# Kernel tuning notes

Hardware: AMD Instinct MI355X
Metric: run time of the kernel (lower is better)

Reference implementation:

```python
import jax, jax.numpy as jnp
import numpy as np

B, T, D_IN = 2048, 26, 512
H = 512          # hidden_size
E = 256          # num_char_embeddings
C = 97           # num_class
S = 32           # num_steps = batch_max_length + 1


def setup_inputs() -> dict:
    key = jax.random.key(0)
    ks = jax.random.split(key, 16)
    sc = lambda n: 1.0 / np.sqrt(n)
    inp = {
        "batch_H": jax.random.normal(ks[0], (B, T, D_IN), jnp.float32),
        "text": jax.random.randint(ks[1], (B, S), 0, C),
        # attention cell params
        "W_i2h": jax.random.normal(ks[2], (H, D_IN), jnp.float32) * sc(D_IN),
        "W_h2h": jax.random.normal(ks[3], (H, H), jnp.float32) * sc(H),
        "b_h2h": jax.random.normal(ks[4], (H,), jnp.float32) * sc(H),
        "w_score": jax.random.normal(ks[5], (1, H), jnp.float32) * sc(H),
        # LSTMCell params (gate order: i, f, g, o)
        "W_ih": jax.random.normal(ks[6], (4 * H, D_IN + E), jnp.float32) * sc(D_IN + E),
        "W_hh": jax.random.normal(ks[7], (4 * H, H), jnp.float32) * sc(H),
        "b_ih": jax.random.normal(ks[8], (4 * H,), jnp.float32) * sc(H),
        "b_hh": jax.random.normal(ks[9], (4 * H,), jnp.float32) * sc(H),
        # generator + char embedding
        "W_gen": jax.random.normal(ks[10], (C, H), jnp.float32) * sc(H),
        "b_gen": jax.random.normal(ks[11], (C,), jnp.float32) * sc(H),
        "emb_table": jax.random.normal(ks[12], (C, E), jnp.float32),
    }
    return inp


def _decode(batch_H, text, W_i2h, W_h2h, b_h2h, w_score,
            W_ih, W_hh, b_ih, b_hh, emb_table):
    # i2h(batch_H) is constant across steps -> hoist out of the loop
    Hp = jnp.einsum('btd,hd->bth', batch_H, W_i2h)          # [B,T,H]
    char_embs = emb_table[text]                              # [B,S,E]
    h0 = jnp.zeros((batch_H.shape[0], H), batch_H.dtype)
    c0 = jnp.zeros_like(h0)

    def step(carry, ce):
        h, c = carry
        ph = h @ W_h2h.T + b_h2h                             # [B,H]
        e = jnp.tanh(Hp + ph[:, None, :]) @ w_score[0]       # [B,T]
        alpha = jax.nn.softmax(e, axis=1)                    # [B,T]
        context = jnp.einsum('bt,btd->bd', alpha, batch_H)   # [B,D_IN]
        x = jnp.concatenate([context, ce], axis=1)           # [B,D_IN+E]
        gates = x @ W_ih.T + b_ih + h @ W_hh.T + b_hh        # [B,4H]
        i, f, g, o = jnp.split(gates, 4, axis=1)
        c_new = jax.nn.sigmoid(f) * c + jax.nn.sigmoid(i) * jnp.tanh(g)
        h_new = jax.nn.sigmoid(o) * jnp.tanh(c_new)
        return (h_new, c_new), h_new

    _, hs = jax.lax.scan(step, (h0, c0), jnp.swapaxes(char_embs, 0, 1))
    return jnp.swapaxes(hs, 0, 1)                            # [B,S,H]


def reference(batch_H, text, W_i2h, W_h2h, b_h2h, w_score,
              W_ih, W_hh, b_ih, b_hh, W_gen, b_gen, emb_table):
    output_hiddens = _decode(batch_H, text, W_i2h, W_h2h, b_h2h, w_score,
                             W_ih, W_hh, b_ih, b_hh, emb_table)
    probs = output_hiddens @ W_gen.T + b_gen                 # [B,S,C]
    return probs
```

## Files before the change

### kernel.cpp

```cpp
#include <hip/hip_runtime.h>

#define BB 2048
#define TT 26
#define DIN 512
#define HH 512
#define EE 256
#define CC 97
#define SS 32
#define G4 2048
#define XK2 1024

typedef unsigned short u16;
typedef __bf16 bf16x8 __attribute__((ext_vector_type(8)));
typedef float f32x4 __attribute__((ext_vector_type(4)));

__device__ __forceinline__ float bf2f(u16 u) {
    return __uint_as_float(((unsigned int)u) << 16);
}
__device__ __forceinline__ u16 f2bf(float f) {
    unsigned int u = __float_as_uint(f);
    u = u + 0x7FFFu + ((u >> 16) & 1u);
    return (u16)(u >> 16);
}
__device__ __forceinline__ float th_f(float x) {
    return 1.0f - 2.0f * __builtin_amdgcn_rcpf(__expf(2.0f * x) + 1.0f);
}
__device__ __forceinline__ float sig_f(float x) {
    return __builtin_amdgcn_rcpf(1.0f + __expf(-x));
}

__device__ __forceinline__ void async16(const u16* g, u16* l) {
    __builtin_amdgcn_global_load_lds(
        (const __attribute__((address_space(1))) unsigned int*)(g),
        (__attribute__((address_space(3))) unsigned int*)(l), 16, 0, 0);
}

__global__ __launch_bounds__(256) void gemm128(
    const u16* __restrict__ A, int lda,
    const u16* __restrict__ W,
    u16* __restrict__ Cout, int ldc, int K)
{
    __shared__ __align__(16) u16 As[128 * 32];
    __shared__ __align__(16) u16 Ws[128 * 32];

    const int tid  = threadIdx.x;
    const int lane = tid & 63;
    const int wave = tid >> 6;
    const int m0 = blockIdx.y * 128;
    const int n0 = blockIdx.x * 128;

    const int srow = tid >> 2;
    const int scol = (tid & 3) * 8;
    const u16* Arow0 = A + (size_t)(m0 + srow) * lda + scol;
    const u16* Arow1 = A + (size_t)(m0 + 64 + srow) * lda + scol;
    const u16* Wrow0 = W + (size_t)(n0 + srow) * K + scol;
    const u16* Wrow1 = W + (size_t)(n0 + 64 + srow) * K + scol;
    u16* dstA0 = As + wave * 512;
    u16* dstA1 = As + 2048 + wave * 512;
    u16* dstW0 = Ws + wave * 512;
    u16* dstW1 = Ws + 2048 + wave * 512;

    const int wm = (wave >> 1) * 64;
    const int wn = (wave & 1) * 64;
    const int fr = lane & 15;
    const int fq = lane >> 4;

    f32x4 acc[4][4];
    #pragma unroll
    for (int i = 0; i < 4; i++)
        #pragma unroll
        for (int j = 0; j < 4; j++)
            #pragma unroll
            for (int r = 0; r < 4; r++) acc[i][j][r] = 0.0f;

    for (int k0 = 0; k0 < K; k0 += 32) {
        async16(Arow0 + k0, dstA0);
        async16(Arow1 + k0, dstA1);
        async16(Wrow0 + k0, dstW0);
        async16(Wrow1 + k0, dstW1);
        __syncthreads();
        bf16x8 af[4], bw[4];
        #pragma unroll
        for (int i = 0; i < 4; i++)
            af[i] = *(const bf16x8*)&As[(wm + i * 16 + fr) * 32 + fq * 8];
        #pragma unroll
        for (int j = 0; j < 4; j++)
            bw[j] = *(const bf16x8*)&Ws[(wn + j * 16 + fr) * 32 + fq * 8];
        #pragma unroll
        for (int i = 0; i < 4; i++)
            #pragma unroll
            for (int j = 0; j < 4; j++)
                acc[i][j] = __builtin_amdgcn_mfma_f32_16x16x32_bf16(
                    af[i], bw[j], acc[i][j], 0, 0, 0);
        __syncthreads();
    }

    #pragma unroll
    for (int j = 0; j < 4; j++) {
        int col = n0 + wn + j * 16 + fr;
        #pragma unroll
        for (int i = 0; i < 4; i++) {
            int row = m0 + wm + i * 16 + fq * 4;
            #pragma unroll
            for (int r = 0; r < 4; r++)
                Cout[(size_t)(row + r) * ldc + col] = f2bf(acc[i][j][r]);
        }
    }
}

__global__ __launch_bounds__(256) void gen128(
    const u16* __restrict__ A,
    const u16* __restrict__ Wg,
    const float* __restrict__ bgen,
    float* __restrict__ out)
{
    __shared__ __align__(16) u16 As[128 * 32];
    __shared__ __align__(16) u16 Ws[128 * 32];

    const int tid  = threadIdx.x;
    const int lane = tid & 63;
    const int wave = tid >> 6;
    const int m0 = blockIdx.y * 128;

    const int srow = tid >> 2;
    const int scol = (tid & 3) * 8;
    const u16* Arow0 = A + (size_t)(m0 + srow) * HH + scol;
    const u16* Arow1 = A + (size_t)(m0 + 64 + srow) * HH + scol;
    const u16* Wrow0 = Wg + (size_t)srow * HH + scol;
    const u16* Wrow1 = Wg + (size_t)(64 + srow) * HH + scol;
    u16* dstA0 = As + wave * 512;
    u16* dstA1 = As + 2048 + wave * 512;
    u16* dstW0 = Ws + wave * 512;
    u16* dstW1 = Ws + 2048 + wave * 512;

    const int wm = (wave >> 1) * 64;
    const int wn = (wave & 1) * 64;
    const int fr = lane & 15;
    const int fq = lane >> 4;

    f32x4 acc[4][4];
    #pragma unroll
    for (int i = 0; i < 4; i++)
        #pragma unroll
        for (int j = 0; j < 4; j++)
            #pragma unroll
            for (int r = 0; r < 4; r++) acc[i][j][r] = 0.0f;

    for (int k0 = 0; k0 < HH; k0 += 32) {
        async16(Arow0 + k0, dstA0);
        async16(Arow1 + k0, dstA1);
        async16(Wrow0 + k0, dstW0);
        async16(Wrow1 + k0, dstW1);
        __syncthreads();
        bf16x8 af[4], bw[4];
        #pragma unroll
        for (int i = 0; i < 4; i++)
            af[i] = *(const bf16x8*)&As[(wm + i * 16 + fr) * 32 + fq * 8];
        #pragma unroll
        for (int j = 0; j < 4; j++)
            bw[j] = *(const bf16x8*)&Ws[(wn + j * 16 + fr) * 32 + fq * 8];
        #pragma unroll
        for (int i = 0; i < 4; i++)
            #pragma unroll
            for (int j = 0; j < 4; j++)
                acc[i][j] = __builtin_amdgcn_mfma_f32_16x16x32_bf16(
                    af[i], bw[j], acc[i][j], 0, 0, 0);
        __syncthreads();
    }

    #pragma unroll
    for (int j = 0; j < 4; j++) {
        int col = wn + j * 16 + fr;
        if (col < CC) {
            float bv = bgen[col];
            #pragma unroll
            for (int i = 0; i < 4; i++) {
                int row = m0 + wm + i * 16 + fq * 4;
                #pragma unroll
                for (int r = 0; r < 4; r++) {
                    int m = row + r;
                    int s = m >> 11, b = m & (BB - 1);
                    out[(size_t)b * (SS * CC) + s * CC + col] = acc[i][j][r] + bv;
                }
            }
        }
    }
}

__global__ __launch_bounds__(256) void gates_lstm(
    const u16* __restrict__ ctx,
    const u16* __restrict__ hprev,
    const u16* __restrict__ Wc,
    const float* __restrict__ bcat,
    const float* __restrict__ P,
    const int* __restrict__ text,
    float* __restrict__ c,
    u16* __restrict__ hnext,
    int s)
{
    __shared__ __align__(16) u16 As[64 * 32];
    __shared__ __align__(16) u16 Ws[128 * 32];
    __shared__ float gsm[64 * 68];
    __shared__ int text_sm[64];

    const int tid  = threadIdx.x;
    const int lane = tid & 63;
    const int wave = tid >> 6;

    int b   = blockIdx.y * gridDim.x + blockIdx.x;
    int xcd = b & 7, loc = b >> 3;
    int by = (xcd & 3) * 8 + (loc & 7);
    int bx = (xcd >> 2) * 8 + (loc >> 3);
    const int m0 = by * 64;
    const int n0 = bx * 128;

    if (tid < 64) text_sm[tid] = text[(m0 + tid) * SS + s];

    const int srow = tid >> 2;
    const int scol = (tid & 3) * 8;
    const u16* Actx  = ctx   + (size_t)(m0 + srow) * 512 + scol;
    const u16* Ahid  = hprev + (size_t)(m0 + srow) * 512 + scol;
    const u16* Wrow0 = Wc + (size_t)(n0 + srow) * XK2 + scol;
    const u16* Wrow1 = Wc + (size_t)(n0 + 64 + srow) * XK2 + scol;
    u16* dstA  = As + wave * 512;
    u16* dstW0 = Ws + wave * 512;
    u16* dstW1 = Ws + 2048 + wave * 512;

    const int wm = (wave & 1) * 32;
    const int wn = (wave >> 1) * 64;
    const int fr = lane & 15;
    const int fq = lane >> 4;

    f32x4 acc[2][4];
    #pragma unroll
    for (int i = 0; i < 2; i++)
        #pragma unroll
        for (int j = 0; j < 4; j++)
            #pragma unroll
            for (int r = 0; r < 4; r++) acc[i][j][r] = 0.0f;

    #pragma unroll
    for (int k0 = 0; k0 < XK2; k0 += 32) {
        const u16* asrc = (k0 < 512) ? (Actx + k0) : (Ahid + (k0 - 512));
        async16(asrc, dstA);
        async16(Wrow0 + k0, dstW0);
        async16(Wrow1 + k0, dstW1);
        __syncthreads();
        bf16x8 af[2], bw[4];
        #pragma unroll
        for (int i = 0; i < 2; i++)
            af[i] = *(const bf16x8*)&As[(wm + i * 16 + fr) * 32 + fq * 8];
        #pragma unroll
        for (int j = 0; j < 4; j++)
            bw[j] = *(const bf16x8*)&Ws[(wn + j * 16 + fr) * 32 + fq * 8];
        #pragma unroll
        for (int i = 0; i < 2; i++)
            #pragma unroll
            for (int j = 0; j < 4; j++)
                acc[i][j] = __builtin_amdgcn_mfma_f32_16x16x32_bf16(
                    af[i], bw[j], acc[i][j], 0, 0, 0);
        __syncthreads();
    }

    #pragma unroll
    for (int p = 0; p < 2; p++) {
        if ((wave >> 1) == p) {
            #pragma unroll
            for (int j = 0; j < 4; j++) {
                int cl = j * 16 + fr;
                #pragma unroll
                for (int i = 0; i < 2; i++) {
                    int rl = wm + i * 16 + fq * 4;
                    #pragma unroll
                    for (int r = 0; r < 4; r++)
                        gsm[(rl + r) * 68 + cl] = acc[i][j][r];
                }
            }
        }
        __syncthreads();
        #pragma unroll
        for (int rr = 0; rr < 4; rr++) {
            int idx = rr * 256 + tid;
            int u = idx & 15, row = idx >> 4;
            int base = row * 68 + 4 * u;
            int hg = (n0 >> 2) + p * 16 + u;
            int c0 = 4 * hg;
            int ch = text_sm[row];
            float4 bc = *(const float4*)(bcat + c0);
            float4 pv = *(const float4*)(P + (size_t)ch * G4 + c0);
            float ig = sig_f(gsm[base]     + bc.x + pv.x);
            float fg = sig_f(gsm[base + 1] + bc.y + pv.y);
            float gg = th_f (gsm[base + 2] + bc.z + pv.z);
            float og = sig_f(gsm[base + 3] + bc.w + pv.w);
            size_t ci = (size_t)(m0 + row) * HH + hg;
            float cn = fg * c[ci] + ig * gg;
            c[ci] = cn;
            hnext[(size_t)(m0 + row) * HH + hg] = f2bf(og * th_f(cn));
        }
        __syncthreads();
    }
}

__global__ __launch_bounds__(256) void gemm64(
    const u16* __restrict__ A, int lda,
    const u16* __restrict__ W, int ldw,
    const float* __restrict__ bias,
    float* __restrict__ Cout, int ldc, int K, int use_bias)
{
    __shared__ __align__(16) u16 As[64][32];
    __shared__ __align__(16) u16 Ws[64][32];

    const int tid  = threadIdx.x;
    const int lane = tid & 63;
    const int wave = tid >> 6;
    const int m0 = blockIdx.y * 64;
    const int n0 = blockIdx.x * 64;
    const int ar = tid >> 2;
    const int ac = (tid & 3) * 8;
    const int wm = (wave >> 1) * 32;
    const int wn = (wave & 1) * 32;
    const int fr = lane & 15;
    const int fq = lane >> 4;

    f32x4 acc[2][2];
    #pragma unroll
    for (int i = 0; i < 2; i++)
        #pragma unroll
        for (int j = 0; j < 2; j++)
            #pragma unroll
            for (int r = 0; r < 4; r++) acc[i][j][r] = 0.0f;

    const u16* Arow = A + (size_t)(m0 + ar) * lda;
    const u16* Wrow = W + (size_t)(n0 + ar) * ldw;

    for (int k0 = 0; k0 < K; k0 += 32) {
        *(uint4*)&As[ar][ac] = *(const uint4*)(Arow + k0 + ac);
        *(uint4*)&Ws[ar][ac] = *(const uint4*)(Wrow + k0 + ac);
        __syncthreads();
        bf16x8 af[2], bw[2];
        #pragma unroll
        for (int mm = 0; mm < 2; mm++)
            af[mm] = *(const bf16x8*)&As[wm + mm * 16 + fr][fq * 8];
        #pragma unroll
        for (int nn = 0; nn < 2; nn++)
            bw[nn] = *(const bf16x8*)&Ws[wn + nn * 16 + fr][fq * 8];
        #pragma unroll
        for (int mm = 0; mm < 2; mm++)
            #pragma unroll
            for (int nn = 0; nn < 2; nn++)
                acc[mm][nn] = __builtin_amdgcn_mfma_f32_16x16x32_bf16(
                    af[mm], bw[nn], acc[mm][nn], 0, 0, 0);
        __syncthreads();
    }

    #pragma unroll
    for (int nn = 0; nn < 2; nn++) {
        int col = n0 + wn + nn * 16 + fr;
        float bv = use_bias ? bias[col] : 0.0f;
        #pragma unroll
        for (int mm = 0; mm < 2; mm++) {
            int row = m0 + wm + mm * 16 + fq * 4;
            #pragma unroll
            for (int r = 0; r < 4; r++)
                Cout[(size_t)(row + r) * ldc + col] = acc[mm][nn][r] + bv;
        }
    }
}

__global__ __launch_bounds__(256) void attn_step(
    const u16* __restrict__ Hp, const float* __restrict__ ph,
    const float* __restrict__ wscore, const u16* __restrict__ bH16,
    u16* __restrict__ ctx)
{
    const int b = blockIdx.x;
    const int tid = threadIdx.x, lane = tid & 63, wave = tid >> 6;
    __shared__ float e_sm[32];
    __shared__ float alpha_sm[32];

    const int h8 = lane * 8;
    float ph_r[8], ws_r[8];
    {
        float4 p0 = *(const float4*)(ph + (size_t)b * HH + h8);
        float4 p1 = *(const float4*)(ph + (size_t)b * HH + h8 + 4);
        ph_r[0]=p0.x; ph_r[1]=p0.y; ph_r[2]=p0.z; ph_r[3]=p0.w;
        ph_r[4]=p1.x; ph_r[5]=p1.y; ph_r[6]=p1.z; ph_r[7]=p1.w;
        float4 w0 = *(const float4*)(wscore + h8);
        float4 w1 = *(const float4*)(wscore + h8 + 4);
        ws_r[0]=w0.x; ws_r[1]=w0.y; ws_r[2]=w0.z; ws_r[3]=w0.w;
        ws_r[4]=w1.x; ws_r[5]=w1.y; ws_r[6]=w1.z; ws_r[7]=w1.w;
    }

    for (int t = wave; t < TT; t += 4) {
        uint4 hv = *(const uint4*)(Hp + ((size_t)b * TT + t) * HH + h8);
        const u16* hu = (const u16*)&hv;
        float sum = 0.0f;
        #pragma unroll
        for (int j = 0; j < 8; j++)
            sum += th_f(bf2f(hu[j]) + ph_r[j]) * ws_r[j];
        #pragma unroll
        for (int off = 32; off > 0; off >>= 1) sum += __shfl_down(sum, off);
        if (lane == 0) e_sm[t] = sum;
    }
    __syncthreads();

    if (tid == 0) {
        float mx = e_sm[0];
        for (int t = 1; t < TT; t++) mx = fmaxf(mx, e_sm[t]);
        float ssum = 0.0f;
        for (int t = 0; t < TT; t++) {
            float ev = __expf(e_sm[t] - mx);
            alpha_sm[t] = ev;
            ssum += ev;
        }
        float inv = 1.0f / ssum;
        for (int t = 0; t < TT; t++) alpha_sm[t] *= inv;
    }
    __syncthreads();

    {
        int d0 = tid * 2;
        float c0 = 0.0f, c1 = 0.0f;
        const u16* bb = bH16 + (size_t)b * TT * DIN + d0;
        #pragma unroll
        for (int t = 0; t < TT; t++) {
            unsigned int v = *(const unsigned int*)(bb + (size_t)t * DIN);
            float a = alpha_sm[t];
            c0 += a * bf2f((u16)(v & 0xffffu));
            c1 += a * bf2f((u16)(v >> 16));
        }
        unsigned int o = (unsigned int)f2bf(c0) | ((unsigned int)f2bf(c1) << 16);
        *(unsigned int*)(ctx + (size_t)b * 512 + d0) = o;
    }
}

__global__ __launch_bounds__(256) void cast_f32_bf16(
    const float* __restrict__ src, u16* __restrict__ dst, int n)
{
    int i = (blockIdx.x * 256 + threadIdx.x) * 4;
    if (i < n) {
        float4 v = *(const float4*)(src + i);
        ushort4 o;
        o.x = f2bf(v.x); o.y = f2bf(v.y); o.z = f2bf(v.z); o.w = f2bf(v.w);
        *(ushort4*)(dst + i) = o;
    }
}

__global__ __launch_bounds__(256) void prep_all(
    const float* __restrict__ W_ih, const float* __restrict__ W_hh,
    const float* __restrict__ b_ih, const float* __restrict__ b_hh,
    const float* __restrict__ b_h2h, const float* __restrict__ emb,
    const float* __restrict__ W_i2h, const float* __restrict__ W_h2h,
    const float* __restrict__ W_gen,
    u16* __restrict__ Wcat, u16* __restrict__ Wce16, u16* __restrict__ emb16,
    u16* __restrict__ Wgen16, u16* __restrict__ Wi2h16, u16* __restrict__ Wh2h16,
    float* __restrict__ bcat, float* __restrict__ cst, u16* __restrict__ hid0,
    float* __restrict__ ph)
{
    int i = blockIdx.x * 256 + threadIdx.x;

    {
        int np = i >> 10, k = i & (XK2 - 1);
        int h = np >> 2, g = np & 3;
        int n = g * HH + h;
        float v = (k < 512) ? W_ih[(size_t)n * (DIN + EE) + k]
                            : W_hh[(size_t)n * HH + (k - 512)];
        Wcat[(size_t)i] = f2bf(v);
    }
    if (i < G4 * EE) {
        int np = i >> 8, e = i & (EE - 1);
        int h = np >> 2, g = np & 3;
        int n = g * HH + h;
        Wce16[i] = f2bf(W_ih[(size_t)n * (DIN + EE) + DIN + e]);
    }
    if (i < 128 * EE) {
        int ch = i >> 8, e = i & (EE - 1);
        emb16[i] = (ch < CC) ? f2bf(emb[(size_t)ch * EE + e]) : (u16)0;
    }
    if (i < 128 * HH) {
        int n = i >> 9, k = i & (HH - 1);
        Wgen16[i] = (n < CC) ? f2bf(W_gen[(size_t)n * HH + k]) : (u16)0;
    }
    if (i < HH * DIN) Wi2h16[i] = f2bf(W_i2h[i]);
    if (i < HH * HH)  Wh2h16[i] = f2bf(W_h2h[i]);
    if (i < G4) {
        int h = i >> 2, g = i & 3;
        int n = g * HH + h;
        bcat[i] = b_ih[n] + b_hh[n];
    }
    if (i < BB * HH) {
        cst[i] = 0.0f;
        hid0[i] = 0;
        ph[i] = b_h2h[i & (HH - 1)];
    }
}

#define BH16_OFF  ((size_t)0)
#define HP_OFF    ((size_t)54525952)
#define HID_OFF   ((size_t)109051904)
#define CTX_OFF   ((size_t)178257920)
#define WCAT_OFF  ((size_t)180355072)
#define WCE_OFF   ((size_t)184549376)
#define EMB16_OFF ((size_t)185597952)
#define WGEN_OFF  ((size_t)185663488)
#define WI2H_OFF  ((size_t)185794560)
#define WH2H_OFF  ((size_t)186318848)
#define BCAT_OFF  ((size_t)186843136)
#define P_OFF     ((size_t)186851328)
#define PH_OFF    ((size_t)187899904)
#define CST_OFF   ((size_t)192094208)

extern "C" void kernel_launch(void* const* d_in, const int* in_sizes, int n_in,
                              void* d_out, int out_size, void* d_ws, size_t ws_size,
                              hipStream_t stream)
{
    const float* batch_H = (const float*)d_in[0];
    const int*   text    = (const int*)d_in[1];
    const float* W_i2h   = (const float*)d_in[2];
    const float* W_h2h   = (const float*)d_in[3];
    const float* b_h2h   = (const float*)d_in[4];
    const float* w_score = (const float*)d_in[5];
    const float* W_ih    = (const float*)d_in[6];
    const float* W_hh    = (const float*)d_in[7];
    const float* b_ih    = (const float*)d_in[8];
    const float* b_hh    = (const float*)d_in[9];
    const float* W_gen   = (const float*)d_in[10];
    const float* b_gen   = (const float*)d_in[11];
    const float* emb     = (const float*)d_in[12];

    char* ws = (char*)d_ws;
    u16*   bH16   = (u16*)(ws + BH16_OFF);
    u16*   Hp     = (u16*)(ws + HP_OFF);
    u16*   hid    = (u16*)(ws + HID_OFF);
    u16*   ctx    = (u16*)(ws + CTX_OFF);
    u16*   Wcat   = (u16*)(ws + WCAT_OFF);
    u16*   Wce16  = (u16*)(ws + WCE_OFF);
    u16*   emb16  = (u16*)(ws + EMB16_OFF);
    u16*   Wgen16 = (u16*)(ws + WGEN_OFF);
    u16*   Wi2h16 = (u16*)(ws + WI2H_OFF);
    u16*   Wh2h16 = (u16*)(ws + WH2H_OFF);
    float* bcat   = (float*)(ws + BCAT_OFF);
    float* P      = (float*)(ws + P_OFF);
    float* ph     = (float*)(ws + PH_OFF);
    float* cst    = (float*)(ws + CST_OFF);
    float* out    = (float*)d_out;

    cast_f32_bf16<<<dim3((BB * TT * DIN / 4 + 255) / 256), 256, 0, stream>>>(
        batch_H, bH16, BB * TT * DIN);
    prep_all<<<dim3((G4 * XK2) / 256), 256, 0, stream>>>(
        W_ih, W_hh, b_ih, b_hh, b_h2h, emb, W_i2h, W_h2h, W_gen,
        Wcat, Wce16, emb16, Wgen16, Wi2h16, Wh2h16, bcat, cst, hid, ph);
    gemm64<<<dim3(G4 / 64, 128 / 64), 256, 0, stream>>>(
        emb16, EE, Wce16, EE, nullptr, P, G4, EE, 0);

    gemm128<<<dim3(HH / 128, (BB * TT) / 128), 256, 0, stream>>>(
        bH16, DIN, Wi2h16, Hp, HH, DIN);

    for (int s = 0; s < SS; s++) {
        u16* hprev = hid + (size_t)s * BB * HH;
        u16* hnext = hid + (size_t)(s + 1) * BB * HH;

        attn_step<<<dim3(BB), 256, 0, stream>>>(Hp, ph, w_score, bH16, ctx);

        gates_lstm<<<dim3(G4 / 128, BB / 64), 256, 0, stream>>>(
            ctx, hprev, Wcat, bcat, P, text, cst, hnext, s);

        gemm64<<<dim3(HH / 64, BB / 64), 256, 0, stream>>>(
            hnext, HH, Wh2h16, HH, b_h2h, ph, HH, HH, 1);
    }

    gen128<<<dim3(1, (SS * BB) / 128), 256, 0, stream>>>(
        hid + (size_t)BB * HH, Wgen16, b_gen, out);
}
```

Measured before the change: 1.818 ms.

## Fuse all decode stages into one persistent kernel with grid barriers

Replaces the roughly 100 per-step kernel launches (attention, gates+LSTM, h2h GEMM per step, plus the setup GEMMs and generator) with a single persistent kernel of 512 blocks. The stages are separated by a software grid barrier built on a hierarchical atomic counter. The attention stage is also restructured so that each wave handles one batch row and keeps the scores and softmax in registers. This removes launch overhead and inter-kernel gaps, at the cost of spin-wait barriers, a 2-blocks-per-CU occupancy requirement for co-residency, and possible deadlock if not all blocks are resident.

```diff
diff --git a/kernel.cpp b/kernel.cpp
--- a/kernel.cpp
+++ b/kernel.cpp
@@ -9,6 +9,7 @@
 #define SS 32
 #define G4 2048
 #define XK2 1024
+#define NBLK 512
 
 typedef unsigned short u16;
 typedef __bf16 bf16x8 __attribute__((ext_vector_type(8)));
@@ -28,408 +29,426 @@
 __device__ __forceinline__ float sig_f(float x) {
     return __builtin_amdgcn_rcpf(1.0f + __expf(-x));
 }
-
 __device__ __forceinline__ void async16(const u16* g, u16* l) {
     __builtin_amdgcn_global_load_lds(
         (const __attribute__((address_space(1))) unsigned int*)(g),
         (__attribute__((address_space(3))) unsigned int*)(l), 16, 0, 0);
 }
 
-__global__ __launch_bounds__(256) void gemm128(
-    const u16* __restrict__ A, int lda,
-    const u16* __restrict__ W,
-    u16* __restrict__ Cout, int ldc, int K)
+__device__ __forceinline__ void gridbar(unsigned* sb, unsigned b, int bid) {
+    __syncthreads();
+    if (threadIdx.x == 0) {
+        __threadfence();
+        int c = bid & 7;
+        unsigned p = atomicAdd(&sb[c * 32], 1u);
+        if (p == (b + 1) * 64 - 1) {
+            unsigned q = atomicAdd(&sb[256], 1u);
+            if (q == (b + 1) * 8 - 1)
+                __hip_atomic_store(&sb[288], b + 1, __ATOMIC_RELEASE,
+                                   __HIP_MEMORY_SCOPE_AGENT);
+        }
+        while (__hip_atomic_load(&sb[288], __ATOMIC_RELAXED,
+                                 __HIP_MEMORY_SCOPE_AGENT) < b + 1)
+            __builtin_amdgcn_s_sleep(2);
+        __threadfence();
+    }
+    __syncthreads();
+}
+
+__global__ void __launch_bounds__(256, 2) persist(
+    const u16* __restrict__ bH16, u16* __restrict__ Hp,
+    u16* __restrict__ hid, u16* __restrict__ ctx,
+    const u16* __restrict__ Wcat, const u16* __restrict__ Wce16,
+    const u16* __restrict__ emb16, const u16* __restrict__ Wgen16,
+    const u16* __restrict__ Wi2h16, const u16* __restrict__ Wh2h16,
+    const float* __restrict__ bcat, float* __restrict__ P,
+    float* __restrict__ ph, float* __restrict__ cst,
+    const int* __restrict__ text, const float* __restrict__ wscore,
+    const float* __restrict__ bh2h, const float* __restrict__ bgen,
+    float* __restrict__ out, unsigned* __restrict__ sb)
 {
-    __shared__ __align__(16) u16 As[128 * 32];
-    __shared__ __align__(16) u16 Ws[128 * 32];
-
+    __shared__ __align__(16) union {
+        struct { u16 As[64*32]; u16 Ws[128*32]; float gsm[64*68]; int txt[64]; } g;
+        struct { u16 As[128*32]; u16 Ws[128*32]; } t;
+        struct { u16 As[64*32]; u16 Ws[64*32]; } s;
+    } sm;
+
+    const int bid  = blockIdx.x;
     const int tid  = threadIdx.x;
     const int lane = tid & 63;
     const int wave = tid >> 6;
-    const int m0 = blockIdx.y * 128;
-    const int n0 = blockIdx.x * 128;
-
     const int srow = tid >> 2;
     const int scol = (tid & 3) * 8;
-    const u16* Arow0 = A + (size_t)(m0 + srow) * lda + scol;
-    const u16* Arow1 = A + (size_t)(m0 + 64 + srow) * lda + scol;
-    const u16* Wrow0 = W + (size_t)(n0 + srow) * K + scol;
-    const u16* Wrow1 = W + (size_t)(n0 + 64 + srow) * K + scol;
-    u16* dstA0 = As + wave * 512;
-    u16* dstA1 = As + 2048 + wave * 512;
-    u16* dstW0 = Ws + wave * 512;
-    u16* dstW1 = Ws + 2048 + wave * 512;
-
-    const int wm = (wave >> 1) * 64;
-    const int wn = (wave & 1) * 64;
-    const int fr = lane & 15;
-    const int fq = lane >> 4;
-
-    f32x4 acc[4][4];
-    #pragma unroll
-    for (int i = 0; i < 4; i++)
+    const int fr   = lane & 15;
+    const int fq   = lane >> 4;
+    unsigned barix = 0;
+
+    float ws_r[8];
+    {
+        float4 w0 = *(const float4*)(wscore + lane * 8);
+        float4 w1 = *(const float4*)(wscore + lane * 8 + 4);
+        ws_r[0]=w0.x; ws_r[1]=w0.y; ws_r[2]=w0.z; ws_r[3]=w0.w;
+        ws_r[4]=w1.x; ws_r[5]=w1.y; ws_r[6]=w1.z; ws_r[7]=w1.w;
+    }
+
+    if (bid < 64) {
+        const int m0 = (bid >> 5) * 64;
+        const int n0 = (bid & 31) * 64;
+        const u16* Arow = emb16 + (size_t)(m0 + srow) * EE + scol;
+        const u16* Wrow = Wce16 + (size_t)(n0 + srow) * EE + scol;
+        u16* dA = sm.s.As + wave * 512;
+        u16* dW = sm.s.Ws + wave * 512;
+        const int wm = (wave >> 1) * 32, wn = (wave & 1) * 32;
+        f32x4 acc[2][2];
         #pragma unroll
-        for (int j = 0; j < 4; j++)
-            #pragma unroll
-            for (int r = 0; r < 4; r++) acc[i][j][r] = 0.0f;
-
-    for (int k0 = 0; k0 < K; k0 += 32) {
-        async16(Arow0 + k0, dstA0);
-        async16(Arow1 + k0, dstA1);
-        async16(Wrow0 + k0, dstW0);
-        async16(Wrow1 + k0, dstW1);
+        for (int i = 0; i < 2; i++)
+            #pragma unroll
+            for (int j = 0; j < 2; j++)
+                #pragma unroll
+                for (int r = 0; r < 4; r++) acc[i][j][r] = 0.0f;
+        for (int k0 = 0; k0 < EE; k0 += 32) {
+            async16(Arow + k0, dA);
+            async16(Wrow + k0, dW);
+            __syncthreads();
+            bf16x8 af[2], bw[2];
+            #pragma unroll
+            for (int i = 0; i < 2; i++)
+                af[i] = *(const bf16x8*)&sm.s.As[(wm + i*16 + fr)*32 + fq*8];
+            #pragma unroll
+            for (int j = 0; j < 2; j++)
+                bw[j] = *(const bf16x8*)&sm.s.Ws[(wn + j*16 + fr)*32 + fq*8];
+            #pragma unroll
+            for (int i = 0; i < 2; i++)
+                #pragma unroll
+                for (int j = 0; j < 2; j++)
+                    acc[i][j] = __builtin_amdgcn_mfma_f32_16x16x32_bf16(
+                        af[i], bw[j], acc[i][j], 0, 0, 0);
+            __syncthreads();
+        }
+        #pragma unroll
+        for (int j = 0; j < 2; j++) {
+            int col = n0 + wn + j * 16 + fr;
+            #pragma unroll
+            for (int i = 0; i < 2; i++) {
+                int row = m0 + wm + i * 16 + fq * 4;
+                #pragma unroll
+                for (int r = 0; r < 4; r++)
+                    P[(size_t)(row + r) * G4 + col] = acc[i][j][r];
+            }
+        }
         __syncthreads();
-        bf16x8 af[4], bw[4];
+    }
+
+    for (int tt = bid; tt < 1664; tt += NBLK) {
+        const int n0 = (tt & 3) * 128;
+        const int m0 = (tt >> 2) * 128;
+        const u16* Arow0 = bH16 + (size_t)(m0 + srow) * DIN + scol;
+        const u16* Arow1 = bH16 + (size_t)(m0 + 64 + srow) * DIN + scol;
+        const u16* Wrow0 = Wi2h16 + (size_t)(n0 + srow) * DIN + scol;
+        const u16* Wrow1 = Wi2h16 + (size_t)(n0 + 64 + srow) * DIN + scol;
+        u16* dA0 = sm.t.As + wave * 512;
+        u16* dA1 = sm.t.As + 2048 + wave * 512;
+        u16* dW0 = sm.t.Ws + wave * 512;
+        u16* dW1 = sm.t.Ws + 2048 + wave * 512;
+        const int wm = (wave >> 1) * 64, wn = (wave & 1) * 64;
+        f32x4 acc[4][4];
         #pragma unroll
         for (int i = 0; i < 4; i++)
-            af[i] = *(const bf16x8*)&As[(wm + i * 16 + fr) * 32 + fq * 8];
+            #pragma unroll
+            for (int j = 0; j < 4; j++)
+                #pragma unroll
+                for (int r = 0; r < 4; r++) acc[i][j][r] = 0.0f;
+        for (int k0 = 0; k0 < DIN; k0 += 32) {
+            async16(Arow0 + k0, dA0);
+            async16(Arow1 + k0, dA1);
+            async16(Wrow0 + k0, dW0);
+            async16(Wrow1 + k0, dW1);
+            __syncthreads();
+            bf16x8 af[4], bw[4];
+            #pragma unroll
+            for (int i = 0; i < 4; i++)
+                af[i] = *(const bf16x8*)&sm.t.As[(wm + i*16 + fr)*32 + fq*8];
+            #pragma unroll
+            for (int j = 0; j < 4; j++)
+                bw[j] = *(const bf16x8*)&sm.t.Ws[(wn + j*16 + fr)*32 + fq*8];
+            #pragma unroll
+            for (int i = 0; i < 4; i++)
+                #pragma unroll
+                for (int j = 0; j < 4; j++)
+                    acc[i][j] = __builtin_amdgcn_mfma_f32_16x16x32_bf16(
+                        af[i], bw[j], acc[i][j], 0, 0, 0);
+            __syncthreads();
+        }
         #pragma unroll
-        for (int j = 0; j < 4; j++)
-            bw[j] = *(const bf16x8*)&Ws[(wn + j * 16 + fr) * 32 + fq * 8];
+        for (int j = 0; j < 4; j++) {
+            int col = n0 + wn + j * 16 + fr;
+            #pragma unroll
+            for (int i = 0; i < 4; i++) {
+                int row = m0 + wm + i * 16 + fq * 4;
+                #pragma unroll
+                for (int r = 0; r < 4; r++)
+                    Hp[(size_t)(row + r) * HH + col] = f2bf(acc[i][j][r]);
+            }
+        }
+        __syncthreads();
+    }
+
+    gridbar(sb, barix++, bid);
+
+    for (int s = 0; s < SS; s++) {
+        const u16* hprev = hid + (size_t)s * BB * HH;
+        u16*       hnext = hid + (size_t)(s + 1) * BB * HH;
+
+        {
+            const int r = bid * 4 + wave;
+            const float* phb = ph + (size_t)r * HH + lane * 8;
+            float pr[8];
+            float4 p0 = *(const float4*)phb;
+            float4 p1 = *(const float4*)(phb + 4);
+            pr[0]=p0.x; pr[1]=p0.y; pr[2]=p0.z; pr[3]=p0.w;
+            pr[4]=p1.x; pr[5]=p1.y; pr[6]=p1.z; pr[7]=p1.w;
+
+            float ev[TT];
+            const u16* hpr = Hp + (size_t)r * TT * HH + lane * 8;
+            #pragma unroll
+            for (int t = 0; t < TT; t++) {
+                uint4 hv = *(const uint4*)(hpr + t * HH);
+                const u16* hu = (const u16*)&hv;
+                float sum = 0.0f;
+                #pragma unroll
+                for (int j = 0; j < 8; j++)
+                    sum += th_f(bf2f(hu[j]) + pr[j]) * ws_r[j];
+                #pragma unroll
+                for (int k = 1; k < 64; k <<= 1)
+                    sum += __shfl_xor(sum, k);
+                ev[t] = sum;
+            }
+            float mx = ev[0];
+            #pragma unroll
+            for (int t = 1; t < TT; t++) mx = fmaxf(mx, ev[t]);
+            float ssum = 0.0f;
+            #pragma unroll
+            for (int t = 0; t < TT; t++) { ev[t] = __expf(ev[t] - mx); ssum += ev[t]; }
+            float inv = 1.0f / ssum;
+
+            float cx[8];
+            #pragma unroll
+            for (int j = 0; j < 8; j++) cx[j] = 0.0f;
+            const u16* bb = bH16 + (size_t)r * TT * DIN + lane * 8;
+            #pragma unroll
+            for (int t = 0; t < TT; t++) {
+                uint4 v = *(const uint4*)(bb + t * DIN);
+                const u16* vu = (const u16*)&v;
+                float a = ev[t] * inv;
+                #pragma unroll
+                for (int j = 0; j < 8; j++) cx[j] += a * bf2f(vu[j]);
+            }
+            u16 o[8];
+            #pragma unroll
+            for (int j = 0; j < 8; j++) o[j] = f2bf(cx[j]);
+            *(uint4*)(ctx + (size_t)r * 512 + lane * 8) = *(const uint4*)o;
+        }
+        gridbar(sb, barix++, bid);
+
+        {
+            int xcd = bid & 7, loc = bid >> 3;
+            int by = (xcd & 3) * 8 + (loc & 7);
+            int bx = (xcd >> 2) * 8 + (loc >> 3);
+            const int m0 = by * 64;
+            const int n0 = bx * 128;
+
+            if (tid < 64) sm.g.txt[tid] = text[(m0 + tid) * SS + s];
+
+            const u16* Actx  = ctx   + (size_t)(m0 + srow) * 512 + scol;
+            const u16* Ahid  = hprev + (size_t)(m0 + srow) * 512 + scol;
+            const u16* Wrow0 = Wcat + (size_t)(n0 + srow) * XK2 + scol;
+            const u16* Wrow1 = Wcat + (size_t)(n0 + 64 + srow) * XK2 + scol;
+            u16* dA  = sm.g.As + wave * 512;
+            u16* dW0 = sm.g.Ws + wave * 512;
+            u16* dW1 = sm.g.Ws + 2048 + wave * 512;
+
+            const int wm = (wave & 1) * 32;
+            const int wn = (wave >> 1) * 64;
+
+            f32x4 acc[2][4];
+            #pragma unroll
+            for (int i = 0; i < 2; i++)
+                #pragma unroll
+                for (int j = 0; j < 4; j++)
+                    #pragma unroll
+                    for (int r = 0; r < 4; r++) acc[i][j][r] = 0.0f;
+
+            #pragma unroll
+            for (int k0 = 0; k0 < XK2; k0 += 32) {
+                const u16* asrc = (k0 < 512) ? (Actx + k0) : (Ahid + (k0 - 512));
+                async16(asrc, dA);
+                async16(Wrow0 + k0, dW0);
+                async16(Wrow1 + k0, dW1);
+                __syncthreads();
+                bf16x8 af[2], bw[4];
+                #pragma unroll
+                for (int i = 0; i < 2; i++)
+                    af[i] = *(const bf16x8*)&sm.g.As[(wm + i*16 + fr)*32 + fq*8];
+                #pragma unroll
+                for (int j = 0; j < 4; j++)
+                    bw[j] = *(const bf16x8*)&sm.g.Ws[(wn + j*16 + fr)*32 + fq*8];
+                #pragma unroll
+                for (int i = 0; i < 2; i++)
+                    #pragma unroll
+                    for (int j = 0; j < 4; j++)
+                        acc[i][j] = __builtin_amdgcn_mfma_f32_16x16x32_bf16(
+                            af[i], bw[j], acc[i][j], 0, 0, 0);
+                __syncthreads();
+            }
+
+            #pragma unroll
+            for (int p = 0; p < 2; p++) {
+                if ((wave >> 1) == p) {
+                    #pragma unroll
+                    for (int j = 0; j < 4; j++) {
+                        int cl = j * 16 + fr;
+                        #pragma unroll
+                        for (int i = 0; i < 2; i++) {
+                            int rl = wm + i * 16 + fq * 4;
+                            #pragma unroll
+                            for (int r = 0; r < 4; r++)
+                                sm.g.gsm[(rl + r) * 68 + cl] = acc[i][j][r];
+                        }
+                    }
+                }
+                __syncthreads();
+                #pragma unroll
+                for (int rr = 0; rr < 4; rr++) {
+                    int idx = rr * 256 + tid;
+                    int u = idx & 15, row = idx >> 4;
+                    int base = row * 68 + 4 * u;
+                    int hg = (n0 >> 2) + p * 16 + u;
+                    int c0i = 4 * hg;
+                    int ch = sm.g.txt[row];
+                    float4 bc = *(const float4*)(bcat + c0i);
+                    float4 pv = *(const float4*)(P + (size_t)ch * G4 + c0i);
+                    float ig = sig_f(sm.g.gsm[base]     + bc.x + pv.x);
+                    float fg = sig_f(sm.g.gsm[base + 1] + bc.y + pv.y);
+                    float gg = th_f (sm.g.gsm[base + 2] + bc.z + pv.z);
+                    float og = sig_f(sm.g.gsm[base + 3] + bc.w + pv.w);
+                    size_t ci = (size_t)(m0 + row) * HH + hg;
+                    float cn = fg * cst[ci] + ig * gg;
+                    cst[ci] = cn;
+                    hnext[(size_t)(m0 + row) * HH + hg] = f2bf(og * th_f(cn));
+                }
+                __syncthreads();
+            }
+        }
+        gridbar(sb, barix++, bid);
+
+        if (bid < 256) {
+            const int n0 = (bid & 7) * 64;
+            const int m0 = (bid >> 3) * 64;
+            const u16* Arow = hnext  + (size_t)(m0 + srow) * HH + scol;
+            const u16* Wrow = Wh2h16 + (size_t)(n0 + srow) * HH + scol;
+            u16* dA = sm.s.As + wave * 512;
+            u16* dW = sm.s.Ws + wave * 512;
+            const int wm = (wave >> 1) * 32, wn = (wave & 1) * 32;
+            f32x4 acc[2][2];
+            #pragma unroll
+            for (int i = 0; i < 2; i++)
+                #pragma unroll
+                for (int j = 0; j < 2; j++)
+                    #pragma unroll
+                    for (int r = 0; r < 4; r++) acc[i][j][r] = 0.0f;
+            for (int k0 = 0; k0 < HH; k0 += 32) {
+                async16(Arow + k0, dA);
+                async16(Wrow + k0, dW);
+                __syncthreads();
+                bf16x8 af[2], bw[2];
+                #pragma unroll
+                for (int i = 0; i < 2; i++)
+                    af[i] = *(const bf16x8*)&sm.s.As[(wm + i*16 + fr)*32 + fq*8];
+                #pragma unroll
+                for (int j = 0; j < 2; j++)
+                    bw[j] = *(const bf16x8*)&sm.s.Ws[(wn + j*16 + fr)*32 + fq*8];
+                #pragma unroll
+                for (int i = 0; i < 2; i++)
+                    #pragma unroll
+                    for (int j = 0; j < 2; j++)
+                        acc[i][j] = __builtin_amdgcn_mfma_f32_16x16x32_bf16(
+                            af[i], bw[j], acc[i][j], 0, 0, 0);
+                __syncthreads();
+            }
+            #pragma unroll
+            for (int j = 0; j < 2; j++) {
+                int col = n0 + wn + j * 16 + fr;
+                float bv = bh2h[col];
+                #pragma unroll
+                for (int i = 0; i < 2; i++) {
+                    int row = m0 + wm + i * 16 + fq * 4;
+                    #pragma unroll
+                    for (int r = 0; r < 4; r++)
+                        ph[(size_t)(row + r) * HH + col] = acc[i][j][r] + bv;
+                }
+            }
+        }
+        gridbar(sb, barix++, bid);
+    }
+
+    {
+        const int m0 = bid * 128;
+        const u16* A = hid + (size_t)BB * HH;
+        const u16* Arow0 = A + (size_t)(m0 + srow) * HH + scol;
+        const u16* Arow1 = A + (size_t)(m0 + 64 + srow) * HH + scol;
+        const u16* Wrow0 = Wgen16 + (size_t)srow * HH + scol;
+        const u16* Wrow1 = Wgen16 + (size_t)(64 + srow) * HH + scol;
+        u16* dA0 = sm.t.As + wave * 512;
+        u16* dA1 = sm.t.As + 2048 + wave * 512;
+        u16* dW0 = sm.t.Ws + wave * 512;
+        u16* dW1 = sm.t.Ws + 2048 + wave * 512;
+        const int wm = (wave >> 1) * 64, wn = (wave & 1) * 64;
+        f32x4 acc[4][4];
         #pragma unroll
         for (int i = 0; i < 4; i++)
             #pragma unroll
             for (int j = 0; j < 4; j++)
-                acc[i][j] = __builtin_amdgcn_mfma_f32_16x16x32_bf16(
-                    af[i], bw[j], acc[i][j], 0, 0, 0);
-        __syncthreads();
-    }
-
-    #pragma unroll
-    for (int j = 0; j < 4; j++) {
-        int col = n0 + wn + j * 16 + fr;
+                #pragma unroll
+                for (int r = 0; r < 4; r++) acc[i][j][r] = 0.0f;
+        for (int k0 = 0; k0 < HH; k0 += 32) {
+            async16(Arow0 + k0, dA0);
+            async16(Arow1 + k0, dA1);
+            async16(Wrow0 + k0, dW0);
+            async16(Wrow1 + k0, dW1);
+            __syncthreads();
+            bf16x8 af[4], bw[4];
+            #pragma unroll
+            for (int i = 0; i < 4; i++)
+                af[i] = *(const bf16x8*)&sm.t.As[(wm + i*16 + fr)*32 + fq*8];
+            #pragma unroll
+            for (int j = 0; j < 4; j++)
+                bw[j] = *(const bf16x8*)&sm.t.Ws[(wn + j*16 + fr)*32 + fq*8];
+            #pragma unroll
+            for (int i = 0; i < 4; i++)
+                #pragma unroll
+                for (int j = 0; j < 4; j++)
+                    acc[i][j] = __builtin_amdgcn_mfma_f32_16x16x32_bf16(
+                        af[i], bw[j], acc[i][j], 0, 0, 0);
+            __syncthreads();
+        }
         #pragma unroll
-        for (int i = 0; i < 4; i++) {
-            int row = m0 + wm + i * 16 + fq * 4;
-            #pragma unroll
-            for (int r = 0; r < 4; r++)
-                Cout[(size_t)(row + r) * ldc + col] = f2bf(acc[i][j][r]);
-        }
-    }
-}
-
-__global__ __launch_bounds__(256) void gen128(
-    const u16* __restrict__ A,
-    const u16* __restrict__ Wg,
-    const float* __restrict__ bgen,
-    float* __restrict__ out)
-{
-    __shared__ __align__(16) u16 As[128 * 32];
-    __shared__ __align__(16) u16 Ws[128 * 32];
-
-    const int tid  = threadIdx.x;
-    const int lane = tid & 63;
-    const int wave = tid >> 6;
-    const int m0 = blockIdx.y * 128;
-
-    const int srow = tid >> 2;
-    const int scol = (tid & 3) * 8;
-    const u16* Arow0 = A + (size_t)(m0 + srow) * HH + scol;
-    const u16* Arow1 = A + (size_t)(m0 + 64 + srow) * HH + scol;
-    const u16* Wrow0 = Wg + (size_t)srow * HH + scol;
-    const u16* Wrow1 = Wg + (size_t)(64 + srow) * HH + scol;
-    u16* dstA0 = As + wave * 512;
-    u16* dstA1 = As + 2048 + wave * 512;
-    u16* dstW0 = Ws + wave * 512;
-    u16* dstW1 = Ws + 2048 + wave * 512;
-
-    const int wm = (wave >> 1) * 64;
-    const int wn = (wave & 1) * 64;
-    const int fr = lane & 15;
-    const int fq = lane >> 4;
-
-    f32x4 acc[4][4];
-    #pragma unroll
-    for (int i = 0; i < 4; i++)
-        #pragma unroll
-        for (int j = 0; j < 4; j++)
-            #pragma unroll
-            for (int r = 0; r < 4; r++) acc[i][j][r] = 0.0f;
-
-    for (int k0 = 0; k0 < HH; k0 += 32) {
-        async16(Arow0 + k0, dstA0);
-        async16(Arow1 + k0, dstA1);
-        async16(Wrow0 + k0, dstW0);
-        async16(Wrow1 + k0, dstW1);
-        __syncthreads();
-        bf16x8 af[4], bw[4];
-        #pragma unroll
-        for (int i = 0; i < 4; i++)
-            af[i] = *(const bf16x8*)&As[(wm + i * 16 + fr) * 32 + fq * 8];
-        #pragma unroll
-        for (int j = 0; j < 4; j++)
-            bw[j] = *(const bf16x8*)&Ws[(wn + j * 16 + fr) * 32 + fq * 8];
-        #pragma unroll
-        for (int i = 0; i < 4; i++)
-            #pragma unroll
-            for (int j = 0; j < 4; j++)
-                acc[i][j] = __builtin_amdgcn_mfma_f32_16x16x32_bf16(
-                    af[i], bw[j], acc[i][j], 0, 0, 0);
-        __syncthreads();
-    }
-
-    #pragma unroll
-    for (int j = 0; j < 4; j++) {
-        int col = wn + j * 16 + fr;
-        if (col < CC) {
-            float bv = bgen[col];
-            #pragma unroll
-            for (int i = 0; i < 4; i++) {
-                int row = m0 + wm + i * 16 + fq * 4;
-                #pragma unroll
-                for (int r = 0; r < 4; r++) {
-                    int m = row + r;
-                    int s = m >> 11, b = m & (BB - 1);
-                    out[(size_t)b * (SS * CC) + s * CC + col] = acc[i][j][r] + bv;
+        for (int j = 0; j < 4; j++) {
+            int col = wn + j * 16 + fr;
+            if (col < CC) {
+                float bv = bgen[col];
+                #pragma unroll
+                for (int i = 0; i < 4; i++) {
+                    int row = m0 + wm + i * 16 + fq * 4;
+                    #pragma unroll
+                    for (int r = 0; r < 4; r++) {
+                        int m = row + r;
+                        int ss = m >> 11, b = m & (BB - 1);
+                        out[(size_t)b * (SS * CC) + ss * CC + col] =
+                            acc[i][j][r] + bv;
+                    }
                 }
             }
         }
-    }
-}
-
-__global__ __launch_bounds__(256) void gates_lstm(
-    const u16* __restrict__ ctx,
-    const u16* __restrict__ hprev,
-    const u16* __restrict__ Wc,
-    const float* __restrict__ bcat,
-    const float* __restrict__ P,
-    const int* __restrict__ text,
-    float* __restrict__ c,
-    u16* __restrict__ hnext,
-    int s)
-{
-    __shared__ __align__(16) u16 As[64 * 32];
-    __shared__ __align__(16) u16 Ws[128 * 32];
-    __shared__ float gsm[64 * 68];
-    __shared__ int text_sm[64];
-
-    const int tid  = threadIdx.x;
-    const int lane = tid & 63;
-    const int wave = tid >> 6;
-
-    int b   = blockIdx.y * gridDim.x + blockIdx.x;
-    int xcd = b & 7, loc = b >> 3;
-    int by = (xcd & 3) * 8 + (loc & 7);
-    int bx = (xcd >> 2) * 8 + (loc >> 3);
-    const int m0 = by * 64;
-    const int n0 = bx * 128;
-
-    if (tid < 64) text_sm[tid] = text[(m0 + tid) * SS + s];
-
-    const int srow = tid >> 2;
-    const int scol = (tid & 3) * 8;
-    const u16* Actx  = ctx   + (size_t)(m0 + srow) * 512 + scol;
-    const u16* Ahid  = hprev + (size_t)(m0 + srow) * 512 + scol;
-    const u16* Wrow0 = Wc + (size_t)(n0 + srow) * XK2 + scol;
-    const u16* Wrow1 = Wc + (size_t)(n0 + 64 + srow) * XK2 + scol;
-    u16* dstA  = As + wave * 512;
-    u16* dstW0 = Ws + wave * 512;
-    u16* dstW1 = Ws + 2048 + wave * 512;
-
-    const int wm = (wave & 1) * 32;
-    const int wn = (wave >> 1) * 64;
-    const int fr = lane & 15;
-    const int fq = lane >> 4;
-
-    f32x4 acc[2][4];
-    #pragma unroll
-    for (int i = 0; i < 2; i++)
-        #pragma unroll
-        for (int j = 0; j < 4; j++)
-            #pragma unroll
-            for (int r = 0; r < 4; r++) acc[i][j][r] = 0.0f;
-
-    #pragma unroll
-    for (int k0 = 0; k0 < XK2; k0 += 32) {
-        const u16* asrc = (k0 < 512) ? (Actx + k0) : (Ahid + (k0 - 512));
-        async16(asrc, dstA);
-        async16(Wrow0 + k0, dstW0);
-        async16(Wrow1 + k0, dstW1);
-        __syncthreads();
-        bf16x8 af[2], bw[4];
-        #pragma unroll
-        for (int i = 0; i < 2; i++)
-            af[i] = *(const bf16x8*)&As[(wm + i * 16 + fr) * 32 + fq * 8];
-        #pragma unroll
-        for (int j = 0; j < 4; j++)
-            bw[j] = *(const bf16x8*)&Ws[(wn + j * 16 + fr) * 32 + fq * 8];
-        #pragma unroll
-        for (int i = 0; i < 2; i++)
-            #pragma unroll
-            for (int j = 0; j < 4; j++)
-                acc[i][j] = __builtin_amdgcn_mfma_f32_16x16x32_bf16(
-                    af[i], bw[j], acc[i][j], 0, 0, 0);
-        __syncthreads();
-    }
-
-    #pragma unroll
-    for (int p = 0; p < 2; p++) {
-        if ((wave >> 1) == p) {
-            #pragma unroll
-            for (int j = 0; j < 4; j++) {
-                int cl = j * 16 + fr;
-                #pragma unroll
-                for (int i = 0; i < 2; i++) {
-                    int rl = wm + i * 16 + fq * 4;
-                    #pragma unroll
-                    for (int r = 0; r < 4; r++)
-                        gsm[(rl + r) * 68 + cl] = acc[i][j][r];
-                }
-            }
-        }
-        __syncthreads();
-        #pragma unroll
-        for (int rr = 0; rr < 4; rr++) {
-            int idx = rr * 256 + tid;
-            int u = idx & 15, row = idx >> 4;
-            int base = row * 68 + 4 * u;
-            int hg = (n0 >> 2) + p * 16 + u;
-            int c0 = 4 * hg;
-            int ch = text_sm[row];
-            float4 bc = *(const float4*)(bcat + c0);
-            float4 pv = *(const float4*)(P + (size_t)ch * G4 + c0);
-            float ig = sig_f(gsm[base]     + bc.x + pv.x);
-            float fg = sig_f(gsm[base + 1] + bc.y + pv.y);
-            float gg = th_f (gsm[base + 2] + bc.z + pv.z);
-            float og = sig_f(gsm[base + 3] + bc.w + pv.w);
-            size_t ci = (size_t)(m0 + row) * HH + hg;
-            float cn = fg * c[ci] + ig * gg;
-            c[ci] = cn;
-            hnext[(size_t)(m0 + row) * HH + hg] = f2bf(og * th_f(cn));
-        }
-        __syncthreads();
-    }
-}
-
-__global__ __launch_bounds__(256) void gemm64(
-    const u16* __restrict__ A, int lda,
-    const u16* __restrict__ W, int ldw,
-    const float* __restrict__ bias,
-    float* __restrict__ Cout, int ldc, int K, int use_bias)
-{
-    __shared__ __align__(16) u16 As[64][32];
-    __shared__ __align__(16) u16 Ws[64][32];
-
-    const int tid  = threadIdx.x;
-    const int lane = tid & 63;
-    const int wave = tid >> 6;
-    const int m0 = blockIdx.y * 64;
-    const int n0 = blockIdx.x * 64;
-    const int ar = tid >> 2;
-    const int ac = (tid & 3) * 8;
-    const int wm = (wave >> 1) * 32;
-    const int wn = (wave & 1) * 32;
-    const int fr = lane & 15;
-    const int fq = lane >> 4;
-
-    f32x4 acc[2][2];
-    #pragma unroll
-    for (int i = 0; i < 2; i++)
-        #pragma unroll
-        for (int j = 0; j < 2; j++)
-            #pragma unroll
-            for (int r = 0; r < 4; r++) acc[i][j][r] = 0.0f;
-
-    const u16* Arow = A + (size_t)(m0 + ar) * lda;
-    const u16* Wrow = W + (size_t)(n0 + ar) * ldw;
-
-    for (int k0 = 0; k0 < K; k0 += 32) {
-        *(uint4*)&As[ar][ac] = *(const uint4*)(Arow + k0 + ac);
-        *(uint4*)&Ws[ar][ac] = *(const uint4*)(Wrow + k0 + ac);
-        __syncthreads();
-        bf16x8 af[2], bw[2];
-        #pragma unroll
-        for (int mm = 0; mm < 2; mm++)
-            af[mm] = *(const bf16x8*)&As[wm + mm * 16 + fr][fq * 8];
-        #pragma unroll
-        for (int nn = 0; nn < 2; nn++)
-            bw[nn] = *(const bf16x8*)&Ws[wn + nn * 16 + fr][fq * 8];
-        #pragma unroll
-        for (int mm = 0; mm < 2; mm++)
-            #pragma unroll
-            for (int nn = 0; nn < 2; nn++)
-                acc[mm][nn] = __builtin_amdgcn_mfma_f32_16x16x32_bf16(
-                    af[mm], bw[nn], acc[mm][nn], 0, 0, 0);
-        __syncthreads();
-    }
-
-    #pragma unroll
-    for (int nn = 0; nn < 2; nn++) {
-        int col = n0 + wn + nn * 16 + fr;
-        float bv = use_bias ? bias[col] : 0.0f;
-        #pragma unroll
-        for (int mm = 0; mm < 2; mm++) {
-            int row = m0 + wm + mm * 16 + fq * 4;
-            #pragma unroll
-            for (int r = 0; r < 4; r++)
-                Cout[(size_t)(row + r) * ldc + col] = acc[mm][nn][r] + bv;
-        }
-    }
-}
-
-__global__ __launch_bounds__(256) void attn_step(
-    const u16* __restrict__ Hp, const float* __restrict__ ph,
-    const float* __restrict__ wscore, const u16* __restrict__ bH16,
-    u16* __restrict__ ctx)
-{
-    const int b = blockIdx.x;
-    const int tid = threadIdx.x, lane = tid & 63, wave = tid >> 6;
-    __shared__ float e_sm[32];
-    __shared__ float alpha_sm[32];
-
-    const int h8 = lane * 8;
-    float ph_r[8], ws_r[8];
-    {
-        float4 p0 = *(const float4*)(ph + (size_t)b * HH + h8);
-        float4 p1 = *(const float4*)(ph + (size_t)b * HH + h8 + 4);
-        ph_r[0]=p0.x; ph_r[1]=p0.y; ph_r[2]=p0.z; ph_r[3]=p0.w;
-        ph_r[4]=p1.x; ph_r[5]=p1.y; ph_r[6]=p1.z; ph_r[7]=p1.w;
-        float4 w0 = *(const float4*)(wscore + h8);
-        float4 w1 = *(const float4*)(wscore + h8 + 4);
-        ws_r[0]=w0.x; ws_r[1]=w0.y; ws_r[2]=w0.z; ws_r[3]=w0.w;
-        ws_r[4]=w1.x; ws_r[5]=w1.y; ws_r[6]=w1.z; ws_r[7]=w1.w;
-    }
-
-    for (int t = wave; t < TT; t += 4) {
-        uint4 hv = *(const uint4*)(Hp + ((size_t)b * TT + t) * HH + h8);
-        const u16* hu = (const u16*)&hv;
-        float sum = 0.0f;
-        #pragma unroll
-        for (int j = 0; j < 8; j++)
-            sum += th_f(bf2f(hu[j]) + ph_r[j]) * ws_r[j];
-        #pragma unroll
-        for (int off = 32; off > 0; off >>= 1) sum += __shfl_down(sum, off);
-        if (lane == 0) e_sm[t] = sum;
-    }
-    __syncthreads();
-
-    if (tid == 0) {
-        float mx = e_sm[0];
-        for (int t = 1; t < TT; t++) mx = fmaxf(mx, e_sm[t]);
-        float ssum = 0.0f;
-        for (int t = 0; t < TT; t++) {
-            float ev = __expf(e_sm[t] - mx);
-            alpha_sm[t] = ev;
-            ssum += ev;
-        }
-        float inv = 1.0f / ssum;
-        for (int t = 0; t < TT; t++) alpha_sm[t] *= inv;
-    }
-    __syncthreads();
-
-    {
-        int d0 = tid * 2;
-        float c0 = 0.0f, c1 = 0.0f;
-        const u16* bb = bH16 + (size_t)b * TT * DIN + d0;
-        #pragma unroll
-        for (int t = 0; t < TT; t++) {
-            unsigned int v = *(const unsigned int*)(bb + (size_t)t * DIN);
-            float a = alpha_sm[t];
-            c0 += a * bf2f((u16)(v & 0xffffu));
-            c1 += a * bf2f((u16)(v >> 16));
-        }
-        unsigned int o = (unsigned int)f2bf(c0) | ((unsigned int)f2bf(c1) << 16);
-        *(unsigned int*)(ctx + (size_t)b * 512 + d0) = o;
     }
 }
 
@@ -454,7 +473,7 @@
     u16* __restrict__ Wcat, u16* __restrict__ Wce16, u16* __restrict__ emb16,
     u16* __restrict__ Wgen16, u16* __restrict__ Wi2h16, u16* __restrict__ Wh2h16,
     float* __restrict__ bcat, float* __restrict__ cst, u16* __restrict__ hid0,
-    float* __restrict__ ph)
+    float* __restrict__ ph, unsigned* __restrict__ sb)
 {
     int i = blockIdx.x * 256 + threadIdx.x;
 
@@ -492,6 +511,7 @@
         hid0[i] = 0;
         ph[i] = b_h2h[i & (HH - 1)];
     }
+    if (i < 320) sb[i] = 0;
 }
 
 #define BH16_OFF  ((size_t)0)
@@ -508,6 +528,7 @@
 #define P_OFF     ((size_t)186851328)
 #define PH_OFF    ((size_t)187899904)
 #define CST_OFF   ((size_t)192094208)
+#define SYNC_OFF  ((size_t)196288512)
 
 extern "C" void kernel_launch(void* const* d_in, const int* in_sizes, int n_in,
                               void* d_out, int out_size, void* d_ws, size_t ws_size,
@@ -542,32 +563,16 @@
     float* P      = (float*)(ws + P_OFF);
     float* ph     = (float*)(ws + PH_OFF);
     float* cst    = (float*)(ws + CST_OFF);
+    unsigned* sb  = (unsigned*)(ws + SYNC_OFF);
     float* out    = (float*)d_out;
 
-    cast_f32_bf16<<<dim3((BB * TT * DIN / 4 + 255) / 256), 256, 0, stream>>>(
+    cast_f32_bf16<<<dim3((BB * TT * DIN / 4) / 256), 256, 0, stream>>>(
         batch_H, bH16, BB * TT * DIN);
     prep_all<<<dim3((G4 * XK2) / 256), 256, 0, stream>>>(
         W_ih, W_hh, b_ih, b_hh, b_h2h, emb, W_i2h, W_h2h, W_gen,
-        Wcat, Wce16, emb16, Wgen16, Wi2h16, Wh2h16, bcat, cst, hid, ph);
-    gemm64<<<dim3(G4 / 64, 128 / 64), 256, 0, stream>>>(
-        emb16, EE, Wce16, EE, nullptr, P, G4, EE, 0);
-
-    gemm128<<<dim3(HH / 128, (BB * TT) / 128), 256, 0, stream>>>(
-        bH16, DIN, Wi2h16, Hp, HH, DIN);
-
-    for (int s = 0; s < SS; s++) {
-        u16* hprev = hid + (size_t)s * BB * HH;
-        u16* hnext = hid + (size_t)(s + 1) * BB * HH;
-
-        attn_step<<<dim3(BB), 256, 0, stream>>>(Hp, ph, w_score, bH16, ctx);
-
-        gates_lstm<<<dim3(G4 / 128, BB / 64), 256, 0, stream>>>(
-            ctx, hprev, Wcat, bcat, P, text, cst, hnext, s);
-
-        gemm64<<<dim3(HH / 64, BB / 64), 256, 0, stream>>>(
-            hnext, HH, Wh2h16, HH, b_h2h, ph, HH, HH, 1);
-    }
-
-    gen128<<<dim3(1, (SS * BB) / 128), 256, 0, stream>>>(
-        hid + (size_t)BB * HH, Wgen16, b_gen, out);
-}
+        Wcat, Wce16, emb16, Wgen16, Wi2h16, Wh2h16, bcat, cst, hid, ph, sb);
+
+    persist<<<dim3(NBLK), 256, 0, stream>>>(
+        bH16, Hp, hid, ctx, Wcat, Wce16, emb16, Wgen16, Wi2h16, Wh2h16,
+        bcat, P, ph, cst, text, w_score, b_h2h, b_gen, out, sb);
+}
```

New measurement: 5.511 ms. 3.03x slower.
